# Optimization experiments

Measured on AMD Instinct MI355X. Metric: run time of the kernel, lower is better.

## Reference

```python
import jax, jax.numpy as jnp
import numpy as np

N = 100000   # nodes
E = 1600000  # edges
D = 128      # input_dim
H = 128      # hidden_dim
O = 128      # output_dim
G = 64       # graphs in batch
BN_EPS = 1e-5


def setup_inputs() -> dict:
    key = jax.random.key(0)
    ks = jax.random.split(key, 32)
    x = jax.random.normal(ks[0], (N, D), jnp.float32)
    edge_index = jax.random.randint(ks[1], (2, E), 0, N, dtype=jnp.int64)
    batch = jnp.sort(jax.random.randint(ks[2], (N,), 0, G, dtype=jnp.int64))

    def lin_w(k, fan_in, fan_out):
        return (jax.random.normal(k, (fan_in, fan_out), jnp.float32) / np.sqrt(fan_in)).astype(jnp.float32)

    def lin_b(k, fan_out):
        return (0.01 * jax.random.normal(k, (fan_out,), jnp.float32)).astype(jnp.float32)

    def bn(k, dim):
        k1, k2, k3, k4 = jax.random.split(k, 4)
        gamma = 1.0 + 0.1 * jax.random.normal(k1, (dim,), jnp.float32)
        beta = 0.1 * jax.random.normal(k2, (dim,), jnp.float32)
        mean = 0.1 * jax.random.normal(k3, (dim,), jnp.float32)
        var = 0.5 + jax.random.uniform(k4, (dim,), jnp.float32)
        return gamma, beta, mean, var

    inp = {
        "x": x, "edge_index": edge_index, "batch": batch,
        "w11": lin_w(ks[3], D, H), "b11": lin_b(ks[4], H),
        "w12": lin_w(ks[5], H, H), "b12": lin_b(ks[6], H),
        "w21": lin_w(ks[7], H, H), "b21": lin_b(ks[8], H),
        "w22": lin_w(ks[9], H, H), "b22": lin_b(ks[10], H),
        "w31": lin_w(ks[11], H, H), "b31": lin_b(ks[12], H),
        "w32": lin_w(ks[13], H, O), "b32": lin_b(ks[14], O),
    }
    g1, be1, m1, v1 = bn(ks[15], H)
    g2, be2, m2, v2 = bn(ks[16], H)
    g3, be3, m3, v3 = bn(ks[17], O)
    inp.update({"bn1_g": g1, "bn1_b": be1, "bn1_m": m1, "bn1_v": v1,
                "bn2_g": g2, "bn2_b": be2, "bn2_m": m2, "bn2_v": v2,
                "bn3_g": g3, "bn3_b": be3, "bn3_m": m3, "bn3_v": v3})
    return inp


def _gin_conv(x, src, dst, wa, ba, wb, bb):
    # sum-aggregate neighbor features: out[i] = x[i] + sum_{(j->i) in E} x[j]  (eps=0)
    agg = jax.ops.segment_sum(x[src], dst, num_segments=N)
    h = x + agg
    # 2-layer MLP: Linear -> ReLU -> Linear
    return jax.nn.relu(h @ wa + ba) @ wb + bb


def _bn_eval(x, g, b, m, v):
    return (x - m) * (g * jax.lax.rsqrt(v + BN_EPS)) + b


def reference(x, edge_index, batch,
              w11, b11, w12, b12, w21, b21, w22, b22, w31, b31, w32, b32,
              bn1_g, bn1_b, bn1_m, bn1_v,
              bn2_g, bn2_b, bn2_m, bn2_v,
              bn3_g, bn3_b, bn3_m, bn3_v):
    src, dst = edge_index[0], edge_index[1]
    h = _gin_conv(x, src, dst, w11, b11, w12, b12)
    h = jax.nn.relu(_bn_eval(h, bn1_g, bn1_b, bn1_m, bn1_v))  # dropout: eval-mode identity
    h = _gin_conv(h, src, dst, w21, b21, w22, b22)
    h = jax.nn.relu(_bn_eval(h, bn2_g, bn2_b, bn2_m, bn2_v))
    h = _gin_conv(h, src, dst, w31, b31, w32, b32)
    h = jax.nn.relu(_bn_eval(h, bn3_g, bn3_b, bn3_m, bn3_v))
    # global mean pool over each graph
    sums = jax.ops.segment_sum(h, batch, num_segments=G)
    counts = jax.ops.segment_sum(jnp.ones((N,), h.dtype), batch, num_segments=G)
    return sums / jnp.maximum(counts, 1.0)[:, None]
```

## Files before the change

### kernel.cpp

```cpp
#include <hip/hip_runtime.h>
#include <hip/hip_bf16.h>
#include <cstdint>

static constexpr int D = 128;
static constexpr int SPANB = 9;
static constexpr int CHUNK = 4096;

typedef __bf16 v8bf __attribute__((ext_vector_type(8)));
typedef float  v4f  __attribute__((ext_vector_type(4)));

__device__ inline float bflo(unsigned u) { return __uint_as_float(u << 16); }
__device__ inline float bfhi(unsigned u) { return __uint_as_float(u & 0xffff0000u); }
__device__ inline unsigned short bfbits(float f) {
    __hip_bfloat16 h = __float2bfloat16(f);
    return *reinterpret_cast<unsigned short*>(&h);
}
__device__ inline unsigned packbf(float a, float b) {
    return (unsigned)bfbits(a) | ((unsigned)bfbits(b) << 16);
}

__global__ __launch_bounds__(256) void prep_kernel(
    const float* __restrict__ w11, const float* __restrict__ w12,
    const float* __restrict__ w21, const float* __restrict__ w22,
    const float* __restrict__ w31, const float* __restrict__ w32,
    __hip_bfloat16* __restrict__ Wp,
    const float* bn1g, const float* bn1b, const float* bn1m, const float* bn1v, const float* lb1,
    const float* bn2g, const float* bn2b, const float* bn2m, const float* bn2v, const float* lb2,
    const float* bn3g, const float* bn3b, const float* bn3m, const float* bn3v, const float* lb3,
    float* sc1, float* sh1, float* sc2, float* sh2, float* sc3, float* sh3,
    const float* __restrict__ x, __hip_bfloat16* __restrict__ xb, long long n8,
    const int* __restrict__ dst, int* __restrict__ blockhist, int nE, int nblk) {
    int b = blockIdx.x, t = threadIdx.x;
    if (b < 48) {
        int idx = b * 256 + t;
        int widx = idx >> 11, r = idx & 2047;
        const float* W = widx == 0 ? w11 : widx == 1 ? w12 : widx == 2 ? w21
                       : widx == 3 ? w22 : widx == 4 ? w31 : w32;
        int l = r & 63, cf = (r >> 6) & 7, ks = r >> 9;
        int k0 = ks * 32 + (l >> 4) * 8, c = cf * 16 + (l & 15);
        unsigned o0 = packbf(W[(k0 + 0) * D + c], W[(k0 + 1) * D + c]);
        unsigned o1 = packbf(W[(k0 + 2) * D + c], W[(k0 + 3) * D + c]);
        unsigned o2 = packbf(W[(k0 + 4) * D + c], W[(k0 + 5) * D + c]);
        unsigned o3 = packbf(W[(k0 + 6) * D + c], W[(k0 + 7) * D + c]);
        reinterpret_cast<uint4*>(Wp + (size_t)idx * 8)[0] = make_uint4(o0, o1, o2, o3);
    } else if (b < 51) {
        if (t < D) {
            int j = b - 48;
            const float *g, *bb, *m, *v, *lb;
            float *sc, *sh;
            if (j == 0)      { g = bn1g; bb = bn1b; m = bn1m; v = bn1v; lb = lb1; sc = sc1; sh = sh1; }
            else if (j == 1) { g = bn2g; bb = bn2b; m = bn2m; v = bn2v; lb = lb2; sc = sc2; sh = sh2; }
            else             { g = bn3g; bb = bn3b; m = bn3m; v = bn3v; lb = lb3; sc = sc3; sh = sh3; }
            float s = g[t] * rsqrtf(v[t] + 1e-5f);
            sc[t] = s;
            sh[t] = (lb[t] - m[t]) * s + bb[t];
        }
    } else if (b < 51 + nblk) {
        __shared__ int h[256];
        h[t] = 0;
        __syncthreads();
        int base = (b - 51) * CHUNK;
#pragma unroll
        for (int i = 0; i < CHUNK / 256; ++i) {
            int e = base + i * 256 + t;
            if (e < nE) atomicAdd(&h[dst[e] >> SPANB], 1);
        }
        __syncthreads();
        blockhist[(b - 51) * 256 + t] = h[t];
    } else {
        long long i = (long long)(b - 51 - nblk) * 256 + t;
        if (i < n8) {
            const float4* f4 = reinterpret_cast<const float4*>(x);
            float4 a = f4[i * 2], bb = f4[i * 2 + 1];
            uint4 o = make_uint4(packbf(a.x, a.y), packbf(a.z, a.w),
                                 packbf(bb.x, bb.y), packbf(bb.z, bb.w));
            reinterpret_cast<uint4*>(xb)[i] = o;
        }
    }
}

__global__ __launch_bounds__(256) void bscan_kernel(int* __restrict__ blockhist,
                                                    int* __restrict__ totals, int nblk) {
    __shared__ int s[256];
    int b = blockIdx.x, t = threadIdx.x;
    int running = 0;
    for (int base = 0; base < nblk; base += 256) {
        int idx = base + t;
        int v = (idx < nblk) ? blockhist[idx * 256 + b] : 0;
        s[t] = v;
        __syncthreads();
#pragma unroll
        for (int off = 1; off < 256; off <<= 1) {
            int add = (t >= off) ? s[t - off] : 0;
            __syncthreads();
            s[t] += add;
            __syncthreads();
        }
        if (idx < nblk) blockhist[idx * 256 + b] = running + s[t] - v;
        int tot = s[255];
        __syncthreads();
        running += tot;
    }
    if (t == 0) totals[b] = running;
}

__global__ void tscan_kernel(const int* __restrict__ totals,
                             int* __restrict__ bucketbase, int nbuk, int nE) {
    __shared__ int s[256];
    int t = threadIdx.x;
    int v = (t < nbuk) ? totals[t] : 0;
    s[t] = v;
    __syncthreads();
#pragma unroll
    for (int off = 1; off < 256; off <<= 1) {
        int add = (t >= off) ? s[t - off] : 0;
        __syncthreads();
        s[t] += add;
        __syncthreads();
    }
    if (t < nbuk) bucketbase[t] = s[t] - v;
    if (t == 0) bucketbase[nbuk] = nE;
}

__global__ __launch_bounds__(256) void fill2_kernel(const int* __restrict__ src,
                                                    const int* __restrict__ dst,
                                                    const int* __restrict__ blockhist,
                                                    const int* __restrict__ bucketbase,
                                                    unsigned* __restrict__ records,
                                                    int nE, int nbuk) {
    __shared__ int cur[256];
    int t = threadIdx.x;
    if (t < nbuk) cur[t] = bucketbase[t] + blockhist[blockIdx.x * 256 + t];
    __syncthreads();
    int base = blockIdx.x * CHUNK;
#pragma unroll
    for (int i = 0; i < CHUNK / 256; ++i) {
        int e = base + i * 256 + t;
        if (e < nE) {
            int d = dst[e], s = src[e];
            int p = atomicAdd(&cur[d >> SPANB], 1);
            records[p] = ((unsigned)s << SPANB) | (unsigned)(d & ((1 << SPANB) - 1));
        }
    }
}

__global__ __launch_bounds__(512) void csr2_kernel(const unsigned* __restrict__ records,
                                                   const int* __restrict__ bucketbase,
                                                   int* __restrict__ rowptr,
                                                   int* __restrict__ col,
                                                   int nN, int nE) {
    __shared__ int cnt[512];
    __shared__ int cur[512];
    int b = blockIdx.x, t = threadIdx.x;
    int node0 = b << SPANB;
    cnt[t] = 0;
    __syncthreads();
    int rbeg = bucketbase[b], rend = bucketbase[b + 1];
    for (int r = rbeg + t; r < rend; r += 512)
        atomicAdd(&cnt[records[r] & ((1 << SPANB) - 1)], 1);
    __syncthreads();
    int v = cnt[t];
#pragma unroll
    for (int off = 1; off < 512; off <<= 1) {
        int add = (t >= off) ? cnt[t - off] : 0;
        __syncthreads();
        cnt[t] += add;
        __syncthreads();
    }
    int pos = rbeg + cnt[t] - v;
    if (node0 + t < nN) rowptr[node0 + t] = pos;
    if (b == 0 && t == 0) rowptr[nN] = nE;
    cur[t] = pos;
    __syncthreads();
    for (int r = rbeg + t; r < rend; r += 512) {
        unsigned rec = records[r];
        int p = atomicAdd(&cur[rec & ((1 << SPANB) - 1)], 1);
        col[p] = (int)(rec >> SPANB);
    }
}

#define ACC8(vv) { a[0]+=bflo(vv.x); a[1]+=bfhi(vv.x); a[2]+=bflo(vv.y); a[3]+=bfhi(vv.y); \
                   a[4]+=bflo(vv.z); a[5]+=bfhi(vv.z); a[6]+=bflo(vv.w); a[7]+=bfhi(vv.w); }

__global__ __launch_bounds__(256) void layer_kernel(
    const __hip_bfloat16* __restrict__ Hin,
    const int* __restrict__ rowptr, const int* __restrict__ col,
    const __hip_bfloat16* __restrict__ WpA, const __hip_bfloat16* __restrict__ WpB,
    const float* __restrict__ b1,
    const float* __restrict__ sc, const float* __restrict__ sh,
    __hip_bfloat16* __restrict__ Hout, int nN) {
    __shared__ __attribute__((aligned(16))) char Sl[64 * 256];
    int t = threadIdx.x;
    int row0 = blockIdx.x * 64;

    {
        int grp = t >> 4, q = t & 15;
        const uint4* h4 = reinterpret_cast<const uint4*>(Hin);
#pragma unroll
        for (int n = 0; n < 4; ++n) {
            int r = grp * 4 + n;
            int node = row0 + r;
            int waddr = r * 256 + ((q * 16) ^ ((r & 7) << 4));
            if (node >= nN) {
                *reinterpret_cast<uint4*>(Sl + waddr) = make_uint4(0, 0, 0, 0);
                continue;
            }
            uint4 u = h4[(size_t)node * 16 + q];
            float a[8];
            a[0] = bflo(u.x); a[1] = bfhi(u.x); a[2] = bflo(u.y); a[3] = bfhi(u.y);
            a[4] = bflo(u.z); a[5] = bfhi(u.z); a[6] = bflo(u.w); a[7] = bfhi(u.w);
            int beg = rowptr[node], end = rowptr[node + 1];
            int j = beg;
            for (; j + 3 < end; j += 4) {
                int s0 = col[j], s1 = col[j + 1], s2 = col[j + 2], s3 = col[j + 3];
                uint4 v0 = h4[(size_t)s0 * 16 + q];
                uint4 v1 = h4[(size_t)s1 * 16 + q];
                uint4 v2 = h4[(size_t)s2 * 16 + q];
                uint4 v3 = h4[(size_t)s3 * 16 + q];
                ACC8(v0); ACC8(v1); ACC8(v2); ACC8(v3);
            }
            for (; j < end; ++j) {
                uint4 v0 = h4[(size_t)col[j] * 16 + q];
                ACC8(v0);
            }
            *reinterpret_cast<uint4*>(Sl + waddr) =
                make_uint4(packbf(a[0], a[1]), packbf(a[2], a[3]),
                           packbf(a[4], a[5]), packbf(a[6], a[7]));
        }
    }
    __syncthreads();

    int w = t >> 6, l = t & 63;
    int q2 = l >> 4, r16 = l & 15;
    int lrow = w * 16 + r16;
    int row = row0 + lrow;
    int swz = (r16 & 7) << 4;
    char* srow = Sl + lrow * 256;
    char* mid = Sl + w * 4096;
    const v8bf* Wa = reinterpret_cast<const v8bf*>(WpA);
    const v8bf* Wb = reinterpret_cast<const v8bf*>(WpB);
    const float4* b14 = reinterpret_cast<const float4*>(b1);
    const float4* sc4 = reinterpret_cast<const float4*>(sc);
    const float4* sh4 = reinterpret_cast<const float4*>(sh);

    v4f acc[8] = {};
#pragma unroll
    for (int ks = 0; ks < 4; ++ks) {
        v8bf bfrag = *reinterpret_cast<v8bf*>(srow + (((ks * 4 + q2) * 16) ^ swz));
#pragma unroll
        for (int cf = 0; cf < 8; ++cf)
            acc[cf] = __builtin_amdgcn_mfma_f32_16x16x32_bf16(
                Wa[(ks * 8 + cf) * 64 + l], bfrag, acc[cf], 0, 0, 0);
    }
    __syncthreads();

#pragma unroll
    for (int cf = 0; cf < 8; ++cf) {
        float4 bb = b14[cf * 4 + q2];
        float e0 = fmaxf(acc[cf][0] + bb.x, 0.f);
        float e1 = fmaxf(acc[cf][1] + bb.y, 0.f);
        float e2 = fmaxf(acc[cf][2] + bb.z, 0.f);
        float e3 = fmaxf(acc[cf][3] + bb.w, 0.f);
        int waddr = r16 * 256 + ((cf * 32 + q2 * 8) ^ swz);
        *reinterpret_cast<uint2*>(mid + waddr) = make_uint2(packbf(e0, e1), packbf(e2, e3));
    }
    __syncthreads();

    v4f acc2[8] = {};
#pragma unroll
    for (int ks = 0; ks < 4; ++ks) {
        v8bf bfrag = *reinterpret_cast<v8bf*>(mid + r16 * 256 + ((ks * 64 + q2 * 16) ^ swz));
#pragma unroll
        for (int cf = 0; cf < 8; ++cf)
            acc2[cf] = __builtin_amdgcn_mfma_f32_16x16x32_bf16(
                Wb[(ks * 8 + cf) * 64 + l], bfrag, acc2[cf], 0, 0, 0);
    }
    if (row < nN) {
#pragma unroll
        for (int cf = 0; cf < 8; ++cf) {
            float4 s0 = sc4[cf * 4 + q2], s1 = sh4[cf * 4 + q2];
            float e0 = fmaxf(acc2[cf][0] * s0.x + s1.x, 0.f);
            float e1 = fmaxf(acc2[cf][1] * s0.y + s1.y, 0.f);
            float e2 = fmaxf(acc2[cf][2] * s0.z + s1.z, 0.f);
            float e3 = fmaxf(acc2[cf][3] * s0.w + s1.w, 0.f);
            *reinterpret_cast<uint2*>(Hout + (size_t)row * D + cf * 16 + q2 * 4) =
                make_uint2(packbf(e0, e1), packbf(e2, e3));
        }
    }
}

__global__ __launch_bounds__(1024) void pool2_kernel(const __hip_bfloat16* __restrict__ h,
                                                     const int* __restrict__ batch,
                                                     float* __restrict__ out, int nN) {
    int g = blockIdx.x;
    int lo, hi;
    {
        int a = 0, b = nN;
        while (a < b) { int mid = (a + b) >> 1; if (batch[mid] < g) a = mid + 1; else b = mid; }
        lo = a;
        b = nN;
        while (a < b) { int mid = (a + b) >> 1; if (batch[mid] < g + 1) a = mid + 1; else b = mid; }
        hi = a;
    }
    int grp = threadIdx.x >> 4;
    int q = threadIdx.x & 15;
    float a[8] = {};
    const uint4* h4 = reinterpret_cast<const uint4*>(h);
    for (int i = lo + grp; i < hi; i += 64) {
        uint4 v = h4[(size_t)i * 16 + q];
        ACC8(v);
    }
    __shared__ float red[64][130];
#pragma unroll
    for (int k = 0; k < 8; ++k) red[grp][q * 8 + k] = a[k];
    __syncthreads();
    int t = threadIdx.x;
    if (t < D) {
        float s = 0.f;
#pragma unroll 8
        for (int r = 0; r < 64; ++r) s += red[r][t];
        out[(size_t)g * D + t] = s / fmaxf((float)(hi - lo), 1.f);
    }
}

extern "C" void kernel_launch(void* const* d_in, const int* in_sizes, int n_in,
                              void* d_out, int out_size, void* d_ws, size_t ws_size,
                              hipStream_t stream) {
    const float* x    = (const float*)d_in[0];
    const int*   ei   = (const int*)d_in[1];
    const int*   batch= (const int*)d_in[2];
    const float* w11 = (const float*)d_in[3];  const float* b11 = (const float*)d_in[4];
    const float* w12 = (const float*)d_in[5];  const float* b12 = (const float*)d_in[6];
    const float* w21 = (const float*)d_in[7];  const float* b21 = (const float*)d_in[8];
    const float* w22 = (const float*)d_in[9];  const float* b22 = (const float*)d_in[10];
    const float* w31 = (const float*)d_in[11]; const float* b31 = (const float*)d_in[12];
    const float* w32 = (const float*)d_in[13]; const float* b32 = (const float*)d_in[14];
    const float* bn1g = (const float*)d_in[15]; const float* bn1b = (const float*)d_in[16];
    const float* bn1m = (const float*)d_in[17]; const float* bn1v = (const float*)d_in[18];
    const float* bn2g = (const float*)d_in[19]; const float* bn2b = (const float*)d_in[20];
    const float* bn2m = (const float*)d_in[21]; const float* bn2v = (const float*)d_in[22];
    const float* bn3g = (const float*)d_in[23]; const float* bn3b = (const float*)d_in[24];
    const float* bn3m = (const float*)d_in[25]; const float* bn3v = (const float*)d_in[26];

    int nN = in_sizes[0] / D;
    int nE = in_sizes[1] / 2;
    int nG = out_size / D;

    const int* srcp = ei;
    const int* dstp = ei + nE;

    size_t NB2 = (size_t)nN * D * sizeof(__hip_bfloat16);
    char* ws = (char*)d_ws;
    __hip_bfloat16* A16 = (__hip_bfloat16*)ws;
    __hip_bfloat16* B16 = (__hip_bfloat16*)(ws + NB2);
    __hip_bfloat16* Wp  = (__hip_bfloat16*)(ws + 2 * NB2);
    size_t wp_bytes = 6 * 2048 * 8 * sizeof(__hip_bfloat16);
    char* auxp = ws + 2 * NB2 + wp_bytes;
    size_t aux_bytes = 16384;
    float* sc1 = (float*)auxp + 0,   *sh1 = (float*)auxp + 128;
    float* sc2 = (float*)auxp + 256, *sh2 = (float*)auxp + 384;
    float* sc3 = (float*)auxp + 512, *sh3 = (float*)auxp + 640;
    int*   bucketbase = (int*)(auxp + (768 + 64) * 4);
    int*   totals     = bucketbase + 300;
    int* rowptr = (int*)(auxp + aux_bytes);
    int* col    = rowptr + (nN + 1);

    unsigned* records = (unsigned*)B16;
    int* blockhist    = (int*)((char*)B16 + (size_t)nE * 4);

    int nbuk = (nN + 511) >> SPANB;
    int nblk = (nE + CHUNK - 1) / CHUNK;
    long long n8 = (long long)nN * D / 8;
    int cvtBlocks = (int)((n8 + 255) / 256);

    prep_kernel<<<51 + nblk + cvtBlocks, 256, 0, stream>>>(
        w11, w12, w21, w22, w31, w32, Wp,
        bn1g, bn1b, bn1m, bn1v, b12,
        bn2g, bn2b, bn2m, bn2v, b22,
        bn3g, bn3b, bn3m, bn3v, b32,
        sc1, sh1, sc2, sh2, sc3, sh3,
        x, A16, n8,
        dstp, blockhist, nE, nblk);

    bscan_kernel<<<nbuk, 256, 0, stream>>>(blockhist, totals, nblk);
    tscan_kernel<<<1, 256, 0, stream>>>(totals, bucketbase, nbuk, nE);
    fill2_kernel<<<nblk, 256, 0, stream>>>(srcp, dstp, blockhist, bucketbase, records, nE, nbuk);
    csr2_kernel<<<nbuk, 512, 0, stream>>>(records, bucketbase, rowptr, col, nN, nE);

    int layerBlocks = (nN + 63) / 64;
    __hip_bfloat16* Wp1 = Wp + 0 * 16384; __hip_bfloat16* Wp2 = Wp + 1 * 16384;
    __hip_bfloat16* Wp3 = Wp + 2 * 16384; __hip_bfloat16* Wp4 = Wp + 3 * 16384;
    __hip_bfloat16* Wp5 = Wp + 4 * 16384; __hip_bfloat16* Wp6 = Wp + 5 * 16384;

    layer_kernel<<<layerBlocks, 256, 0, stream>>>(A16, rowptr, col, Wp1, Wp2, b11, sc1, sh1, B16, nN);
    layer_kernel<<<layerBlocks, 256, 0, stream>>>(B16, rowptr, col, Wp3, Wp4, b21, sc2, sh2, A16, nN);
    layer_kernel<<<layerBlocks, 256, 0, stream>>>(A16, rowptr, col, Wp5, Wp6, b31, sc3, sh3, B16, nN);

    pool2_kernel<<<nG, 1024, 0, stream>>>(B16, batch, (float*)d_out, nN);
}
```

Measured before the change: 330.3 us.

## Use single-wavefront blocks of 32 rows in GIN layer kernel, dropping barriers

Each layer block is now one 64-thread wavefront handling 32 nodes, so all __syncthreads barriers between gather, MLP and epilogue go away. Each wave runs two 16-row MFMA tiles that share each weight fragment load, halving weight traffic per row. The output is staged through LDS and written as coalesced 16-byte rows. In exchange each thread gathers 8 nodes serially, with less latency hiding per block, and holds twice the accumulators, which raises register pressure.

```diff
diff --git a/kernel.cpp b/kernel.cpp
--- a/kernel.cpp
+++ b/kernel.cpp
@@ -182,23 +182,22 @@
 #define ACC8(vv) { a[0]+=bflo(vv.x); a[1]+=bfhi(vv.x); a[2]+=bflo(vv.y); a[3]+=bfhi(vv.y); \
                    a[4]+=bflo(vv.z); a[5]+=bfhi(vv.z); a[6]+=bflo(vv.w); a[7]+=bfhi(vv.w); }
 
-__global__ __launch_bounds__(256) void layer_kernel(
+__global__ __launch_bounds__(64) void layer_kernel(
     const __hip_bfloat16* __restrict__ Hin,
     const int* __restrict__ rowptr, const int* __restrict__ col,
     const __hip_bfloat16* __restrict__ WpA, const __hip_bfloat16* __restrict__ WpB,
     const float* __restrict__ b1,
     const float* __restrict__ sc, const float* __restrict__ sh,
     __hip_bfloat16* __restrict__ Hout, int nN) {
-    __shared__ __attribute__((aligned(16))) char Sl[64 * 256];
+    __shared__ __attribute__((aligned(16))) char Sl[32 * 256];
     int t = threadIdx.x;
-    int row0 = blockIdx.x * 64;
+    int row0 = blockIdx.x * 32;
 
     {
         int grp = t >> 4, q = t & 15;
         const uint4* h4 = reinterpret_cast<const uint4*>(Hin);
-#pragma unroll
-        for (int n = 0; n < 4; ++n) {
-            int r = grp * 4 + n;
+        for (int n = 0; n < 8; ++n) {
+            int r = grp * 8 + n;
             int node = row0 + r;
             int waddr = r * 256 + ((q * 16) ^ ((r & 7) << 4));
             if (node >= nN) {
@@ -228,63 +227,81 @@
                            packbf(a[4], a[5]), packbf(a[6], a[7]));
         }
     }
-    __syncthreads();
-
-    int w = t >> 6, l = t & 63;
+
+    int l = t;
     int q2 = l >> 4, r16 = l & 15;
-    int lrow = w * 16 + r16;
-    int row = row0 + lrow;
     int swz = (r16 & 7) << 4;
-    char* srow = Sl + lrow * 256;
-    char* mid = Sl + w * 4096;
+    char* srowA = Sl + r16 * 256;
+    char* srowB = Sl + (16 + r16) * 256;
     const v8bf* Wa = reinterpret_cast<const v8bf*>(WpA);
     const v8bf* Wb = reinterpret_cast<const v8bf*>(WpB);
     const float4* b14 = reinterpret_cast<const float4*>(b1);
     const float4* sc4 = reinterpret_cast<const float4*>(sc);
     const float4* sh4 = reinterpret_cast<const float4*>(sh);
 
-    v4f acc[8] = {};
+    v4f acc[2][8] = {};
 #pragma unroll
     for (int ks = 0; ks < 4; ++ks) {
-        v8bf bfrag = *reinterpret_cast<v8bf*>(srow + (((ks * 4 + q2) * 16) ^ swz));
-#pragma unroll
-        for (int cf = 0; cf < 8; ++cf)
-            acc[cf] = __builtin_amdgcn_mfma_f32_16x16x32_bf16(
-                Wa[(ks * 8 + cf) * 64 + l], bfrag, acc[cf], 0, 0, 0);
-    }
-    __syncthreads();
-
-#pragma unroll
-    for (int cf = 0; cf < 8; ++cf) {
-        float4 bb = b14[cf * 4 + q2];
-        float e0 = fmaxf(acc[cf][0] + bb.x, 0.f);
-        float e1 = fmaxf(acc[cf][1] + bb.y, 0.f);
-        float e2 = fmaxf(acc[cf][2] + bb.z, 0.f);
-        float e3 = fmaxf(acc[cf][3] + bb.w, 0.f);
-        int waddr = r16 * 256 + ((cf * 32 + q2 * 8) ^ swz);
-        *reinterpret_cast<uint2*>(mid + waddr) = make_uint2(packbf(e0, e1), packbf(e2, e3));
-    }
-    __syncthreads();
-
-    v4f acc2[8] = {};
+        v8bf bA = *reinterpret_cast<v8bf*>(srowA + (((ks * 4 + q2) * 16) ^ swz));
+        v8bf bB = *reinterpret_cast<v8bf*>(srowB + (((ks * 4 + q2) * 16) ^ swz));
+#pragma unroll
+        for (int cf = 0; cf < 8; ++cf) {
+            v8bf wa = Wa[(ks * 8 + cf) * 64 + l];
+            acc[0][cf] = __builtin_amdgcn_mfma_f32_16x16x32_bf16(wa, bA, acc[0][cf], 0, 0, 0);
+            acc[1][cf] = __builtin_amdgcn_mfma_f32_16x16x32_bf16(wa, bB, acc[1][cf], 0, 0, 0);
+        }
+    }
+#pragma unroll
+    for (int half = 0; half < 2; ++half) {
+        char* base = Sl + half * 4096;
+#pragma unroll
+        for (int cf = 0; cf < 8; ++cf) {
+            float4 bb = b14[cf * 4 + q2];
+            float e0 = fmaxf(acc[half][cf][0] + bb.x, 0.f);
+            float e1 = fmaxf(acc[half][cf][1] + bb.y, 0.f);
+            float e2 = fmaxf(acc[half][cf][2] + bb.z, 0.f);
+            float e3 = fmaxf(acc[half][cf][3] + bb.w, 0.f);
+            int waddr = r16 * 256 + ((cf * 32 + q2 * 8) ^ swz);
+            *reinterpret_cast<uint2*>(base + waddr) = make_uint2(packbf(e0, e1), packbf(e2, e3));
+        }
+    }
+
+    v4f acc2[2][8] = {};
 #pragma unroll
     for (int ks = 0; ks < 4; ++ks) {
-        v8bf bfrag = *reinterpret_cast<v8bf*>(mid + r16 * 256 + ((ks * 64 + q2 * 16) ^ swz));
-#pragma unroll
-        for (int cf = 0; cf < 8; ++cf)
-            acc2[cf] = __builtin_amdgcn_mfma_f32_16x16x32_bf16(
-                Wb[(ks * 8 + cf) * 64 + l], bfrag, acc2[cf], 0, 0, 0);
-    }
-    if (row < nN) {
+        v8bf bA = *reinterpret_cast<v8bf*>(Sl + r16 * 256 + ((ks * 64 + q2 * 16) ^ swz));
+        v8bf bB = *reinterpret_cast<v8bf*>(Sl + 4096 + r16 * 256 + ((ks * 64 + q2 * 16) ^ swz));
+#pragma unroll
+        for (int cf = 0; cf < 8; ++cf) {
+            v8bf wb = Wb[(ks * 8 + cf) * 64 + l];
+            acc2[0][cf] = __builtin_amdgcn_mfma_f32_16x16x32_bf16(wb, bA, acc2[0][cf], 0, 0, 0);
+            acc2[1][cf] = __builtin_amdgcn_mfma_f32_16x16x32_bf16(wb, bB, acc2[1][cf], 0, 0, 0);
+        }
+    }
+#pragma unroll
+    for (int half = 0; half < 2; ++half) {
+        char* base = Sl + half * 4096;
 #pragma unroll
         for (int cf = 0; cf < 8; ++cf) {
             float4 s0 = sc4[cf * 4 + q2], s1 = sh4[cf * 4 + q2];
-            float e0 = fmaxf(acc2[cf][0] * s0.x + s1.x, 0.f);
-            float e1 = fmaxf(acc2[cf][1] * s0.y + s1.y, 0.f);
-            float e2 = fmaxf(acc2[cf][2] * s0.z + s1.z, 0.f);
-            float e3 = fmaxf(acc2[cf][3] * s0.w + s1.w, 0.f);
-            *reinterpret_cast<uint2*>(Hout + (size_t)row * D + cf * 16 + q2 * 4) =
-                make_uint2(packbf(e0, e1), packbf(e2, e3));
+            float e0 = fmaxf(acc2[half][cf][0] * s0.x + s1.x, 0.f);
+            float e1 = fmaxf(acc2[half][cf][1] * s0.y + s1.y, 0.f);
+            float e2 = fmaxf(acc2[half][cf][2] * s0.z + s1.z, 0.f);
+            float e3 = fmaxf(acc2[half][cf][3] * s0.w + s1.w, 0.f);
+            int waddr = r16 * 256 + ((cf * 32 + q2 * 8) ^ swz);
+            *reinterpret_cast<uint2*>(base + waddr) = make_uint2(packbf(e0, e1), packbf(e2, e3));
+        }
+    }
+
+    {
+        int q = t & 15;
+        for (int i = 0; i < 8; ++i) {
+            int r = (t >> 4) * 8 + i;
+            int grow = row0 + r;
+            if (grow < nN) {
+                uint4 v = *reinterpret_cast<uint4*>(Sl + r * 256 + ((q * 16) ^ ((r & 7) << 4)));
+                reinterpret_cast<uint4*>(Hout + (size_t)grow * D)[q] = v;
+            }
         }
     }
 }
@@ -387,14 +404,14 @@
     fill2_kernel<<<nblk, 256, 0, stream>>>(srcp, dstp, blockhist, bucketbase, records, nE, nbuk);
     csr2_kernel<<<nbuk, 512, 0, stream>>>(records, bucketbase, rowptr, col, nN, nE);
 
-    int layerBlocks = (nN + 63) / 64;
+    int layerBlocks = (nN + 31) / 32;
     __hip_bfloat16* Wp1 = Wp + 0 * 16384; __hip_bfloat16* Wp2 = Wp + 1 * 16384;
     __hip_bfloat16* Wp3 = Wp + 2 * 16384; __hip_bfloat16* Wp4 = Wp + 3 * 16384;
     __hip_bfloat16* Wp5 = Wp + 4 * 16384; __hip_bfloat16* Wp6 = Wp + 5 * 16384;
 
-    layer_kernel<<<layerBlocks, 256, 0, stream>>>(A16, rowptr, col, Wp1, Wp2, b11, sc1, sh1, B16, nN);
-    layer_kernel<<<layerBlocks, 256, 0, stream>>>(B16, rowptr, col, Wp3, Wp4, b21, sc2, sh2, A16, nN);
-    layer_kernel<<<layerBlocks, 256, 0, stream>>>(A16, rowptr, col, Wp5, Wp6, b31, sc3, sh3, B16, nN);
+    layer_kernel<<<layerBlocks, 64, 0, stream>>>(A16, rowptr, col, Wp1, Wp2, b11, sc1, sh1, B16, nN);
+    layer_kernel<<<layerBlocks, 64, 0, stream>>>(B16, rowptr, col, Wp3, Wp4, b21, sc2, sh2, A16, nN);
+    layer_kernel<<<layerBlocks, 64, 0, stream>>>(A16, rowptr, col, Wp5, Wp6, b31, sc3, sh3, B16, nN);
 
     pool2_kernel<<<nG, 1024, 0, stream>>>(B16, batch, (float*)d_out, nN);
 }
```

Measured after the change: 451.2 us. 36.6% more time.

## Split fused GIN layer into separate aggregation and MLP kernels

Applied to the files above, without the earlier changes.

Unfuses each layer into an aggregation kernel that gathers neighbour sums into a new bf16 scratch buffer, and an MLP kernel that reads that buffer. The aggregation now runs with one node per 16-lane group across many small blocks, which should balance irregular degrees and improve latency hiding. The MLP kernel stages weights in shared memory and writes output with coalesced 16-byte stores through a swizzled shared tile. In exchange the aggregated features make an extra round trip through global memory each layer, and there are twice as many launches.

```diff
diff --git a/kernel.cpp b/kernel.cpp
--- a/kernel.cpp
+++ b/kernel.cpp
@@ -182,78 +182,81 @@
 #define ACC8(vv) { a[0]+=bflo(vv.x); a[1]+=bfhi(vv.x); a[2]+=bflo(vv.y); a[3]+=bfhi(vv.y); \
                    a[4]+=bflo(vv.z); a[5]+=bfhi(vv.z); a[6]+=bflo(vv.w); a[7]+=bfhi(vv.w); }
 
-__global__ __launch_bounds__(256) void layer_kernel(
-    const __hip_bfloat16* __restrict__ Hin,
-    const int* __restrict__ rowptr, const int* __restrict__ col,
-    const __hip_bfloat16* __restrict__ WpA, const __hip_bfloat16* __restrict__ WpB,
+__global__ __launch_bounds__(256) void agg_kernel(const __hip_bfloat16* __restrict__ h,
+                                                  __hip_bfloat16* __restrict__ S,
+                                                  const int* __restrict__ rowptr,
+                                                  const int* __restrict__ col, int nN) {
+    int node = blockIdx.x * 16 + (threadIdx.x >> 4);
+    if (node >= nN) return;
+    int q = threadIdx.x & 15;
+    const uint4* h4 = reinterpret_cast<const uint4*>(h);
+    uint4 u = h4[(size_t)node * 16 + q];
+    float a[8];
+    a[0] = bflo(u.x); a[1] = bfhi(u.x); a[2] = bflo(u.y); a[3] = bfhi(u.y);
+    a[4] = bflo(u.z); a[5] = bfhi(u.z); a[6] = bflo(u.w); a[7] = bfhi(u.w);
+    int beg = rowptr[node], end = rowptr[node + 1];
+    int j = beg;
+    for (; j + 3 < end; j += 4) {
+        int s0 = col[j], s1 = col[j + 1], s2 = col[j + 2], s3 = col[j + 3];
+        uint4 v0 = h4[(size_t)s0 * 16 + q];
+        uint4 v1 = h4[(size_t)s1 * 16 + q];
+        uint4 v2 = h4[(size_t)s2 * 16 + q];
+        uint4 v3 = h4[(size_t)s3 * 16 + q];
+        ACC8(v0); ACC8(v1); ACC8(v2); ACC8(v3);
+    }
+    for (; j < end; ++j) {
+        uint4 v0 = h4[(size_t)col[j] * 16 + q];
+        ACC8(v0);
+    }
+    uint4 o = make_uint4(packbf(a[0], a[1]), packbf(a[2], a[3]),
+                         packbf(a[4], a[5]), packbf(a[6], a[7]));
+    reinterpret_cast<uint4*>(S)[(size_t)node * 16 + q] = o;
+}
+
+__global__ __launch_bounds__(256) void mlp3_kernel(
+    const __hip_bfloat16* __restrict__ S,
+    const __hip_bfloat16* __restrict__ WpA,
+    const __hip_bfloat16* __restrict__ WpB,
     const float* __restrict__ b1,
     const float* __restrict__ sc, const float* __restrict__ sh,
-    __hip_bfloat16* __restrict__ Hout, int nN) {
-    __shared__ __attribute__((aligned(16))) char Sl[64 * 256];
+    __hip_bfloat16* __restrict__ out, int nN) {
+    __shared__ __attribute__((aligned(16))) char Wl[32768];
+    __shared__ __attribute__((aligned(16))) char Ml[4][4096];
     int t = threadIdx.x;
-    int row0 = blockIdx.x * 64;
-
-    {
-        int grp = t >> 4, q = t & 15;
-        const uint4* h4 = reinterpret_cast<const uint4*>(Hin);
-#pragma unroll
-        for (int n = 0; n < 4; ++n) {
-            int r = grp * 4 + n;
-            int node = row0 + r;
-            int waddr = r * 256 + ((q * 16) ^ ((r & 7) << 4));
-            if (node >= nN) {
-                *reinterpret_cast<uint4*>(Sl + waddr) = make_uint4(0, 0, 0, 0);
-                continue;
-            }
-            uint4 u = h4[(size_t)node * 16 + q];
-            float a[8];
-            a[0] = bflo(u.x); a[1] = bfhi(u.x); a[2] = bflo(u.y); a[3] = bfhi(u.y);
-            a[4] = bflo(u.z); a[5] = bfhi(u.z); a[6] = bflo(u.w); a[7] = bfhi(u.w);
-            int beg = rowptr[node], end = rowptr[node + 1];
-            int j = beg;
-            for (; j + 3 < end; j += 4) {
-                int s0 = col[j], s1 = col[j + 1], s2 = col[j + 2], s3 = col[j + 3];
-                uint4 v0 = h4[(size_t)s0 * 16 + q];
-                uint4 v1 = h4[(size_t)s1 * 16 + q];
-                uint4 v2 = h4[(size_t)s2 * 16 + q];
-                uint4 v3 = h4[(size_t)s3 * 16 + q];
-                ACC8(v0); ACC8(v1); ACC8(v2); ACC8(v3);
-            }
-            for (; j < end; ++j) {
-                uint4 v0 = h4[(size_t)col[j] * 16 + q];
-                ACC8(v0);
-            }
-            *reinterpret_cast<uint4*>(Sl + waddr) =
-                make_uint4(packbf(a[0], a[1]), packbf(a[2], a[3]),
-                           packbf(a[4], a[5]), packbf(a[6], a[7]));
-        }
-    }
-    __syncthreads();
-
     int w = t >> 6, l = t & 63;
     int q2 = l >> 4, r16 = l & 15;
-    int lrow = w * 16 + r16;
-    int row = row0 + lrow;
-    int swz = (r16 & 7) << 4;
-    char* srow = Sl + lrow * 256;
-    char* mid = Sl + w * 4096;
-    const v8bf* Wa = reinterpret_cast<const v8bf*>(WpA);
-    const v8bf* Wb = reinterpret_cast<const v8bf*>(WpB);
+    int row0 = blockIdx.x * 64 + w * 16;
+    int row = row0 + r16;
+    int ar = row < nN ? row : nN - 1;
+
+    v8bf bfrag[4];
+#pragma unroll
+    for (int ks = 0; ks < 4; ++ks)
+        bfrag[ks] = *reinterpret_cast<const v8bf*>(S + (size_t)ar * D + ks * 32 + q2 * 8);
+
+    uint4* wl = reinterpret_cast<uint4*>(Wl);
+    const uint4* wa4 = reinterpret_cast<const uint4*>(WpA);
+    const uint4* wb4 = reinterpret_cast<const uint4*>(WpB);
+
+#pragma unroll
+    for (int i = 0; i < 8; ++i) wl[i * 256 + t] = wa4[i * 256 + t];
+    __syncthreads();
+
+    const v8bf* wv = reinterpret_cast<const v8bf*>(Wl);
     const float4* b14 = reinterpret_cast<const float4*>(b1);
     const float4* sc4 = reinterpret_cast<const float4*>(sc);
     const float4* sh4 = reinterpret_cast<const float4*>(sh);
+    char* mid = Ml[w];
+    int swz = (r16 & 7) << 4;
 
     v4f acc[8] = {};
 #pragma unroll
     for (int ks = 0; ks < 4; ++ks) {
-        v8bf bfrag = *reinterpret_cast<v8bf*>(srow + (((ks * 4 + q2) * 16) ^ swz));
 #pragma unroll
         for (int cf = 0; cf < 8; ++cf)
             acc[cf] = __builtin_amdgcn_mfma_f32_16x16x32_bf16(
-                Wa[(ks * 8 + cf) * 64 + l], bfrag, acc[cf], 0, 0, 0);
-    }
-    __syncthreads();
-
+                wv[(ks * 8 + cf) * 64 + l], bfrag[ks], acc[cf], 0, 0, 0);
+    }
 #pragma unroll
     for (int cf = 0; cf < 8; ++cf) {
         float4 bb = b14[cf * 4 + q2];
@@ -266,25 +269,39 @@
     }
     __syncthreads();
 
+#pragma unroll
+    for (int i = 0; i < 8; ++i) wl[i * 256 + t] = wb4[i * 256 + t];
+    __syncthreads();
+
     v4f acc2[8] = {};
 #pragma unroll
     for (int ks = 0; ks < 4; ++ks) {
-        v8bf bfrag = *reinterpret_cast<v8bf*>(mid + r16 * 256 + ((ks * 64 + q2 * 16) ^ swz));
+        v8bf mfrag = *reinterpret_cast<v8bf*>(mid + r16 * 256 + ((ks * 64 + q2 * 16) ^ swz));
 #pragma unroll
         for (int cf = 0; cf < 8; ++cf)
             acc2[cf] = __builtin_amdgcn_mfma_f32_16x16x32_bf16(
-                Wb[(ks * 8 + cf) * 64 + l], bfrag, acc2[cf], 0, 0, 0);
-    }
-    if (row < nN) {
-#pragma unroll
-        for (int cf = 0; cf < 8; ++cf) {
-            float4 s0 = sc4[cf * 4 + q2], s1 = sh4[cf * 4 + q2];
-            float e0 = fmaxf(acc2[cf][0] * s0.x + s1.x, 0.f);
-            float e1 = fmaxf(acc2[cf][1] * s0.y + s1.y, 0.f);
-            float e2 = fmaxf(acc2[cf][2] * s0.z + s1.z, 0.f);
-            float e3 = fmaxf(acc2[cf][3] * s0.w + s1.w, 0.f);
-            *reinterpret_cast<uint2*>(Hout + (size_t)row * D + cf * 16 + q2 * 4) =
-                make_uint2(packbf(e0, e1), packbf(e2, e3));
+                wv[(ks * 8 + cf) * 64 + l], mfrag, acc2[cf], 0, 0, 0);
+    }
+#pragma unroll
+    for (int cf = 0; cf < 8; ++cf) {
+        float4 s0 = sc4[cf * 4 + q2], s1 = sh4[cf * 4 + q2];
+        float e0 = fmaxf(acc2[cf][0] * s0.x + s1.x, 0.f);
+        float e1 = fmaxf(acc2[cf][1] * s0.y + s1.y, 0.f);
+        float e2 = fmaxf(acc2[cf][2] * s0.z + s1.z, 0.f);
+        float e3 = fmaxf(acc2[cf][3] * s0.w + s1.w, 0.f);
+        int waddr = r16 * 256 + ((cf * 32 + q2 * 8) ^ swz);
+        *reinterpret_cast<uint2*>(mid + waddr) = make_uint2(packbf(e0, e1), packbf(e2, e3));
+    }
+    {
+        int q = l & 15;
+#pragma unroll
+        for (int i = 0; i < 4; ++i) {
+            int r = (l >> 4) * 4 + i;
+            int grow = row0 + r;
+            if (grow < nN) {
+                uint4 v = *reinterpret_cast<uint4*>(mid + r * 256 + ((q * 16) ^ ((r & 7) << 4)));
+                reinterpret_cast<uint4*>(out + (size_t)grow * D)[q] = v;
+            }
         }
     }
 }
@@ -353,9 +370,10 @@
     char* ws = (char*)d_ws;
     __hip_bfloat16* A16 = (__hip_bfloat16*)ws;
     __hip_bfloat16* B16 = (__hip_bfloat16*)(ws + NB2);
-    __hip_bfloat16* Wp  = (__hip_bfloat16*)(ws + 2 * NB2);
+    __hip_bfloat16* S16 = (__hip_bfloat16*)(ws + 2 * NB2);
+    __hip_bfloat16* Wp  = (__hip_bfloat16*)(ws + 3 * NB2);
     size_t wp_bytes = 6 * 2048 * 8 * sizeof(__hip_bfloat16);
-    char* auxp = ws + 2 * NB2 + wp_bytes;
+    char* auxp = ws + 3 * NB2 + wp_bytes;
     size_t aux_bytes = 16384;
     float* sc1 = (float*)auxp + 0,   *sh1 = (float*)auxp + 128;
     float* sc2 = (float*)auxp + 256, *sh2 = (float*)auxp + 384;
@@ -365,8 +383,8 @@
     int* rowptr = (int*)(auxp + aux_bytes);
     int* col    = rowptr + (nN + 1);
 
-    unsigned* records = (unsigned*)B16;
-    int* blockhist    = (int*)((char*)B16 + (size_t)nE * 4);
+    unsigned* records = (unsigned*)S16;
+    int* blockhist    = (int*)((char*)S16 + (size_t)nE * 4);
 
     int nbuk = (nN + 511) >> SPANB;
     int nblk = (nE + CHUNK - 1) / CHUNK;
@@ -387,14 +405,20 @@
     fill2_kernel<<<nblk, 256, 0, stream>>>(srcp, dstp, blockhist, bucketbase, records, nE, nbuk);
     csr2_kernel<<<nbuk, 512, 0, stream>>>(records, bucketbase, rowptr, col, nN, nE);
 
-    int layerBlocks = (nN + 63) / 64;
+    int aggBlocks = (nN + 15) / 16;
+    int mlpBlocks = (nN + 63) / 64;
     __hip_bfloat16* Wp1 = Wp + 0 * 16384; __hip_bfloat16* Wp2 = Wp + 1 * 16384;
     __hip_bfloat16* Wp3 = Wp + 2 * 16384; __hip_bfloat16* Wp4 = Wp + 3 * 16384;
     __hip_bfloat16* Wp5 = Wp + 4 * 16384; __hip_bfloat16* Wp6 = Wp + 5 * 16384;
 
-    layer_kernel<<<layerBlocks, 256, 0, stream>>>(A16, rowptr, col, Wp1, Wp2, b11, sc1, sh1, B16, nN);
-    layer_kernel<<<layerBlocks, 256, 0, stream>>>(B16, rowptr, col, Wp3, Wp4, b21, sc2, sh2, A16, nN);
-    layer_kernel<<<layerBlocks, 256, 0, stream>>>(A16, rowptr, col, Wp5, Wp6, b31, sc3, sh3, B16, nN);
+    agg_kernel<<<aggBlocks, 256, 0, stream>>>(A16, S16, rowptr, col, nN);
+    mlp3_kernel<<<mlpBlocks, 256, 0, stream>>>(S16, Wp1, Wp2, b11, sc1, sh1, B16, nN);
+
+    agg_kernel<<<aggBlocks, 256, 0, stream>>>(B16, S16, rowptr, col, nN);
+    mlp3_kernel<<<mlpBlocks, 256, 0, stream>>>(S16, Wp3, Wp4, b21, sc2, sh2, A16, nN);
+
+    agg_kernel<<<aggBlocks, 256, 0, stream>>>(A16, S16, rowptr, col, nN);
+    mlp3_kernel<<<mlpBlocks, 256, 0, stream>>>(S16, Wp5, Wp6, b31, sc3, sh3, B16, nN);
 
     pool2_kernel<<<nG, 1024, 0, stream>>>(B16, batch, (float*)d_out, nN);
 }
```

Result: faster. 303.5 us (-8.1%).
